# Optimization experiments

Hardware: AMD Instinct MI355X
Metric: run time of the kernel (lower is better)

## Reference

```python
import jax, jax.numpy as jnp
import numpy as np

N, E, T = 10000, 160000, 1200000
D, DM, H, L, Z = 256, 64, 1024, 3, 100


def setup_inputs() -> dict:
    key = jax.random.key(0)
    ks = jax.random.split(key, 24)
    rn = lambda k, shp, s: (s * jax.random.normal(k, shp)).astype(jnp.float32)
    return {
        'atomic_number': jax.random.randint(ks[0], (N,), 1, Z),
        'g_src': jax.random.randint(ks[1], (E,), 0, N),
        'g_dst': jax.random.randint(ks[2], (E,), 0, N),
        't_src': jax.random.randint(ks[3], (T,), 0, E),
        't_dst': jax.random.randint(ks[4], (T,), 0, E),
        'r': rn(ks[5], (E, 3), 1.5),  # bond displacement vectors, |r| ~ 2.4 A
        'atom_emb': rn(ks[6], (Z, D), 0.05),
        'Wsrc': rn(ks[7], (L, D, DM), 0.05), 'bsrc': rn(ks[8], (L, DM), 0.05),
        'Wdst': rn(ks[9], (L, D, DM), 0.05), 'bdst': rn(ks[10], (L, DM), 0.05),
        'Wedge': rn(ks[11], (L, D, DM), 0.05), 'bedge': rn(ks[12], (L, DM), 0.05),
        'attn': rn(ks[13], (L, DM), 0.05),
        'W1': rn(ks[14], (L, DM, H), 0.05), 'b1': rn(ks[15], (L, H), 0.05),
        'W2': rn(ks[16], (L, H, D), 0.05), 'b2': rn(ks[17], (L, D), 0.05),
        'Wfc': rn(ks[18], (D, 1), 0.05), 'bfc': rn(ks[19], (1,), 0.05),
    }


def _forward(atomic_number, g_src, g_dst, t_src, t_dst, r, atom_emb,
             Wsrc, bsrc, Wdst, bdst, Wedge, bedge, attn, W1, b1, W2, b2, Wfc, bfc):
    n_nodes = atomic_number.shape[0]
    n_edges = r.shape[0]
    d_model = atom_emb.shape[1]
    channels = attn.shape[-1]

    # atom embedding + RBF bond encoding (vmin=0, vmax=8, bins=d_model)
    x = atom_emb[atomic_number]                       # [N, D]
    bondlength = jnp.linalg.norm(r, axis=1)           # [E]
    centers = jnp.linspace(0.0, 8.0, d_model)
    gamma = 1.0 / (centers[1] - centers[0]) ** 2
    y = jnp.exp(-gamma * (bondlength[:, None] - centers[None, :]) ** 2)  # [E, D]

    # angular (Chebyshev) features on triplet graph t; t.ndata['r'] = g.edata['r']
    rnorm = -r / bondlength[:, None]                  # [E, 3]
    cos_jik = jnp.sum(rnorm[t_src] * rnorm[t_dst], axis=1)  # [T]
    kc = jnp.arange(channels, dtype=cos_jik.dtype)
    theta = jnp.arccos(jnp.clip(cos_jik, -1.0, 1.0))
    z_jik = jnp.cos(kc[None, :] * theta[:, None])     # [T, C] Chebyshev T_k(cos)

    node_idx = g_dst[t_dst]                           # triplet -> destination atom

    for l in range(Wsrc.shape[0]):
        xj = x @ Wsrc[l] + bsrc[l]                    # [N, DM]
        xi = x @ Wdst[l] + bdst[l]                    # [N, DM]
        xij = xj[g_src] + xi[g_dst] + (y @ Wedge[l] + bedge[l])  # [E, DM]

        e_jik = jax.nn.silu(z_jik + xij[t_src] + xij[t_dst])     # [T, DM]
        logit = jnp.sum(e_jik * attn[l], axis=-1)                # [T]
        # edge_softmax grouped by destination bond (t_dst)
        m = jax.ops.segment_max(logit, t_dst, num_segments=n_edges)
        ex = jnp.exp(logit - m[t_dst])
        den = jax.ops.segment_sum(ex, t_dst, num_segments=n_edges)
        a = ex / den[t_dst]                                      # [T]

        # scatter attended messages to destination atoms
        ft = jax.ops.segment_sum(a[:, None] * xij[t_src], node_idx,
                                 num_segments=n_nodes)           # [N, DM]
        # feedforward: DM -> 4*D -> D
        x = jax.nn.silu(ft @ W1[l] + b1[l]) @ W2[l] + b2[l]      # [N, D]

    atomwise_energy = x @ Wfc + bfc                   # [N, 1]
    return jnp.squeeze(jnp.mean(atomwise_energy))     # AvgPooling, eV/atom


def reference(atomic_number, g_src, g_dst, t_src, t_dst, r, atom_emb,
              Wsrc, bsrc, Wdst, bdst, Wedge, bedge, attn, W1, b1, W2, b2, Wfc, bfc):
    return _forward(atomic_number, g_src, g_dst, t_src, t_dst, r, atom_emb,
                    Wsrc, bsrc, Wdst, bdst, Wedge, bedge, attn, W1, b1, W2, b2, Wfc, bfc)
```

## Files before the change

kernel.cpp:

```cpp
#include <hip/hip_runtime.h>
#include <math.h>


#define DM 64
#define DMODEL 256
#define HDIM 1024
#define WPAD 264

#define BSH 9
#define NBMAX 320
#define CAPB 4608

typedef unsigned short bf16_t;
typedef __attribute__((ext_vector_type(8))) short s8v;
typedef __attribute__((ext_vector_type(4))) float f4;

__device__ __forceinline__ bf16_t f2bf(float f) {
    unsigned int u = __float_as_uint(f);
    return (bf16_t)((u + 0x7FFFu + ((u >> 16) & 1u)) >> 16);
}
__device__ __forceinline__ float bf_lo(unsigned int u) {
    return __uint_as_float(u << 16);
}
__device__ __forceinline__ float bf_hi(unsigned int u) {
    return __uint_as_float(u & 0xFFFF0000u);
}
__device__ __forceinline__ float bf2f(bf16_t v) {
    return __uint_as_float((unsigned int)v << 16);
}
__device__ __forceinline__ float silu_f(float u) {
    return u * __builtin_amdgcn_rcpf(1.f + __expf(-u));
}

__global__ void k_embed(const int* __restrict__ an, const float* __restrict__ emb,
                        bf16_t* __restrict__ x) {
    int n = blockIdx.x;
    int d = threadIdx.x;
    x[n * DMODEL + d] = f2bf(emb[an[n] * DMODEL + d]);
}

__global__ void k_edge_geom(const float* __restrict__ r, float* __restrict__ bl,
                            float* __restrict__ rn, int E) {
    int e = blockIdx.x * blockDim.x + threadIdx.x;
    if (e >= E) return;
    float a = r[e * 3 + 0], b = r[e * 3 + 1], c = r[e * 3 + 2];
    float l = sqrtf(a * a + b * b + c * c);
    bl[e] = l;
    float inv = 1.0f / l;
    rn[e * 3 + 0] = a * inv;
    rn[e * 3 + 1] = b * inv;
    rn[e * 3 + 2] = c * inv;
}

__global__ void k_hist(const int* __restrict__ idx, int* __restrict__ cnt, int M) {
    int t = blockIdx.x * blockDim.x + threadIdx.x;
    if (t < M) atomicAdd(&cnt[idx[t]], 1);
}

__global__ __launch_bounds__(256) void k_scan_part(
    const int* __restrict__ cnt, int* __restrict__ bsum, int M) {
    __shared__ int sm[4];
    int tid = threadIdx.x;
    int i = blockIdx.x * 256 + tid;
    int v = (i < M) ? cnt[i] : 0;
    for (int off = 32; off > 0; off >>= 1) v += __shfl_xor(v, off, 64);
    if ((tid & 63) == 0) sm[tid >> 6] = v;
    __syncthreads();
    if (tid == 0) bsum[blockIdx.x] = sm[0] + sm[1] + sm[2] + sm[3];
}

__global__ __launch_bounds__(1024) void k_scan_mid(int* __restrict__ bsum, int nb) {
    __shared__ int sm[1024];
    int tid = threadIdx.x;
    int v = (tid < nb) ? bsum[tid] : 0;
    sm[tid] = v;
    __syncthreads();
    for (int off = 1; off < 1024; off <<= 1) {
        int u = (tid >= off) ? sm[tid - off] : 0;
        __syncthreads();
        sm[tid] += u;
        __syncthreads();
    }
    if (tid < nb) bsum[tid] = sm[tid] - v;
}

__global__ __launch_bounds__(256) void k_scan_final(
    int* __restrict__ cnt, const int* __restrict__ bsum,
    int* __restrict__ rowp, int M, int total) {
    __shared__ int sm[256];
    int tid = threadIdx.x;
    int i = blockIdx.x * 256 + tid;
    int v = (i < M) ? cnt[i] : 0;
    sm[tid] = v;
    __syncthreads();
    for (int off = 1; off < 256; off <<= 1) {
        int u = (tid >= off) ? sm[tid - off] : 0;
        __syncthreads();
        sm[tid] += u;
        __syncthreads();
    }
    if (i < M) {
        rowp[i] = bsum[blockIdx.x] + sm[tid] - v;
        cnt[i] = 0;
    }
    if (i == 0) rowp[M] = total;
}


__global__ __launch_bounds__(512) void k_bhist(
    const int* __restrict__ td, int* __restrict__ gbcnt, int T, int NB) {
    __shared__ int h[NBMAX];
    int tid = threadIdx.x;
    for (int i = tid; i < NBMAX; i += 512) h[i] = 0;
    __syncthreads();
    int t0 = blockIdx.x * 4096;
    #pragma unroll
    for (int i = 0; i < 8; ++i) {
        int t = t0 + tid + i * 512;
        if (t < T) atomicAdd(&h[td[t] >> BSH], 1);
    }
    __syncthreads();
    for (int b = tid; b < NB; b += 512)
        if (h[b]) atomicAdd(&gbcnt[b], h[b]);
}

__global__ __launch_bounds__(512) void k_bscan(
    const int* __restrict__ gbcnt, int* __restrict__ bbase, int NB, int total) {
    __shared__ int sm[512];
    int tid = threadIdx.x;
    int v = (tid < NB) ? gbcnt[tid] : 0;
    sm[tid] = v;
    __syncthreads();
    for (int off = 1; off < 512; off <<= 1) {
        int u = (tid >= off) ? sm[tid - off] : 0;
        __syncthreads();
        sm[tid] += u;
        __syncthreads();
    }
    if (tid < NB) bbase[tid] = sm[tid] - v;
    if (tid == 0) bbase[NB] = total;
}

__global__ __launch_bounds__(512) void k_passA(
    const int* __restrict__ ts, const int* __restrict__ td,
    const float* __restrict__ rn, const int* __restrict__ bbase,
    int* __restrict__ bcur, int2* __restrict__ ipair, float* __restrict__ idv,
    int T, int NB) {
    __shared__ int   std_[4096];
    __shared__ int   ssrc[4096];
    __shared__ float sdv[4096];
    __shared__ int lbcnt[NBMAX], lbase[NBMAX], lpos[NBMAX], lgst[NBMAX],
                   lbb[NBMAX];
    __shared__ int ssc[512];
    int tid = threadIdx.x;
    int t0 = blockIdx.x * 4096;
    int total = min(4096, T - t0);
    for (int i = tid; i < NBMAX; i += 512) lbcnt[i] = 0;
    for (int i = tid; i < NB; i += 512) lbb[i] = bbase[i];
    __syncthreads();
    int   mtd[8], msrc[8];
    float md[8];
    #pragma unroll
    for (int i = 0; i < 8; ++i) {
        int idx = tid + i * 512;
        mtd[i] = -1;
        if (idx < total) {
            int t = t0 + idx;
            int a = ts[t], b = td[t];
            float d = rn[a * 3 + 0] * rn[b * 3 + 0]
                    + rn[a * 3 + 1] * rn[b * 3 + 1]
                    + rn[a * 3 + 2] * rn[b * 3 + 2];
            d = fminf(1.0f, fmaxf(-1.0f, d));
            mtd[i] = b; msrc[i] = a; md[i] = d;
            atomicAdd(&lbcnt[b >> BSH], 1);
        }
    }
    __syncthreads();
    int v = (tid < NB) ? lbcnt[tid] : 0;
    ssc[tid] = v;
    __syncthreads();
    for (int off = 1; off < 512; off <<= 1) {
        int u = (tid >= off) ? ssc[tid - off] : 0;
        __syncthreads();
        ssc[tid] += u;
        __syncthreads();
    }
    if (tid < NB) {
        int ex = ssc[tid] - v;
        lbase[tid] = ex;
        lpos[tid] = ex;
    }
    __syncthreads();
    #pragma unroll
    for (int i = 0; i < 8; ++i) {
        if (mtd[i] >= 0) {
            int bin = mtd[i] >> BSH;
            int p = atomicAdd(&lpos[bin], 1);
            std_[p] = mtd[i]; ssrc[p] = msrc[i]; sdv[p] = md[i];
        }
    }
    __syncthreads();
    for (int b = tid; b < NB; b += 512)
        if (lbcnt[b]) lgst[b] = atomicAdd(&bcur[b], lbcnt[b]);
    __syncthreads();
    for (int j = tid; j < total; j += 512) {
        int bin = std_[j] >> BSH;
        int dest = lbb[bin] + lgst[bin] + (j - lbase[bin]);
        ipair[dest] = make_int2(std_[j], ssrc[j]);
        idv[dest] = sdv[j];
    }
}

__global__ __launch_bounds__(512) void k_passB(
    const int2* __restrict__ ipair, const float* __restrict__ idv,
    const int* __restrict__ bbase, int2* __restrict__ packed,
    int* __restrict__ rowp, int E, int T) {
    __shared__ int2 spk[CAPB];
    __shared__ int hcnt[512], lcur[512], ssc[512];
    int tid = threadIdx.x;
    int b = blockIdx.x;
    int ibeg = bbase[b], iend = bbase[b + 1];
    int nb = iend - ibeg;
    int e0 = b << BSH;
    hcnt[tid] = 0;
    __syncthreads();
    for (int j = ibeg + tid; j < iend; j += 512)
        atomicAdd(&hcnt[ipair[j].x - e0], 1);
    __syncthreads();
    int v = hcnt[tid];
    ssc[tid] = v;
    __syncthreads();
    for (int off = 1; off < 512; off <<= 1) {
        int u = (tid >= off) ? ssc[tid - off] : 0;
        __syncthreads();
        ssc[tid] += u;
        __syncthreads();
    }
    int excl = ssc[tid] - v;
    lcur[tid] = excl;
    int e = e0 + tid;
    if (e < E) rowp[e] = ibeg + excl;
    if (b == 0 && tid == 0) rowp[E] = T;
    __syncthreads();
    bool staged = (nb <= CAPB);
    for (int j = ibeg + tid; j < iend; j += 512) {
        int2 pr = ipair[j];
        int pos = atomicAdd(&lcur[pr.x - e0], 1);
        int2 out = make_int2(pr.y, __float_as_int(idv[j]));
        if (staged) spk[pos] = out;
        else packed[ibeg + pos] = out;
    }
    __syncthreads();
    if (staged)
        for (int j = tid; j < nb; j += 512) packed[ibeg + j] = spk[j];
}

__global__ void k_escatter(const int* __restrict__ gd, const int* __restrict__ erowp,
                           int* __restrict__ cursor, int* __restrict__ epos, int E) {
    int e = blockIdx.x * blockDim.x + threadIdx.x;
    if (e >= E) return;
    int n = gd[e];
    int pos = erowp[n] + atomicAdd(&cursor[n], 1);
    epos[e] = pos;
}

__global__ __launch_bounds__(256) void k_deghist(
    const int* __restrict__ rowp, int* __restrict__ dcnt, int E) {
    __shared__ int h[256];
    int tid = threadIdx.x;
    h[tid] = 0;
    __syncthreads();
    int e = blockIdx.x * 256 + tid;
    if (e < E) {
        int d = rowp[e + 1] - rowp[e];
        if (d > 255) d = 255;
        atomicAdd(&h[d], 1);
    }
    __syncthreads();
    if (h[tid]) atomicAdd(&dcnt[tid], h[tid]);
}

__global__ __launch_bounds__(256) void k_degscatter(
    const int* __restrict__ rowp, const int* __restrict__ doff,
    int* __restrict__ dcur, int* __restrict__ eperm, int E) {
    __shared__ int lcnt[256];
    __shared__ int base[256];
    int tid = threadIdx.x;
    lcnt[tid] = 0;
    __syncthreads();
    int e = blockIdx.x * 256 + tid;
    int d = 0, rk = 0;
    if (e < E) {
        d = rowp[e + 1] - rowp[e];
        if (d > 255) d = 255;
        rk = atomicAdd(&lcnt[d], 1);
    }
    __syncthreads();
    if (lcnt[tid]) base[tid] = atomicAdd(&dcur[tid], lcnt[tid]);
    __syncthreads();
    if (e < E) eperm[E - 1 - (doff[d] + base[d] + rk)] = e;
}

__global__ __launch_bounds__(256) void k_castT(
    const float* __restrict__ src0, bf16_t* __restrict__ dst0, int K, int Nn) {
    __shared__ float tile[32][33];
    const float* src = src0 + (size_t)blockIdx.z * K * Nn;
    bf16_t* dst = dst0 + (size_t)blockIdx.z * K * Nn;
    int k0 = blockIdx.x * 32, n0 = blockIdx.y * 32;
    int tx = threadIdx.x & 31, ty = threadIdx.x >> 5;
    #pragma unroll
    for (int i = 0; i < 4; ++i) {
        int row = ty + i * 8;
        tile[row][tx] = src[(size_t)(k0 + row) * Nn + n0 + tx];
    }
    __syncthreads();
    #pragma unroll
    for (int i = 0; i < 4; ++i) {
        int row = ty + i * 8;
        dst[(size_t)(n0 + row) * K + k0 + tx] = f2bf(tile[tx][row]);
    }
}

__global__ __launch_bounds__(256) void k_node_proj(
    const bf16_t* __restrict__ xb,
    const bf16_t* __restrict__ Wst, const float* __restrict__ bs,
    const bf16_t* __restrict__ Wdt, const float* __restrict__ bd,
    bf16_t* __restrict__ xs, bf16_t* __restrict__ xd, int N) {
    __shared__ bf16_t wsl[64 * WPAD];
    __shared__ bf16_t wdl[64 * WPAD];
    int tid = threadIdx.x;
    for (int i = tid; i < 2048; i += 256) {
        int row = i >> 5, inw = i & 31;
        *(uint4*)&wsl[row * WPAD + inw * 8] =
            *(const uint4*)&Wst[(size_t)row * DMODEL + inw * 8];
        *(uint4*)&wdl[row * WPAD + inw * 8] =
            *(const uint4*)&Wdt[(size_t)row * DMODEL + inw * 8];
    }
    __syncthreads();
    int w = tid >> 6, lane = tid & 63;
    int col = lane & 15, quad = lane >> 4;
    int m0 = blockIdx.x * 64 + w * 16;
    f4 as[4] = {{0.f,0.f,0.f,0.f},{0.f,0.f,0.f,0.f},
                {0.f,0.f,0.f,0.f},{0.f,0.f,0.f,0.f}};
    f4 ad[4] = {{0.f,0.f,0.f,0.f},{0.f,0.f,0.f,0.f},
                {0.f,0.f,0.f,0.f},{0.f,0.f,0.f,0.f}};
    #pragma unroll
    for (int k0 = 0; k0 < DMODEL; k0 += 32) {
        s8v a = *(const s8v*)&xb[(size_t)(m0 + col) * DMODEL + k0 + quad * 8];
        #pragma unroll
        for (int t = 0; t < 4; ++t) {
            s8v b1v = *(const s8v*)&wsl[(t * 16 + col) * WPAD + k0 + quad * 8];
            as[t] = __builtin_amdgcn_mfma_f32_16x16x32_bf16(a, b1v, as[t], 0, 0, 0);
            s8v b2v = *(const s8v*)&wdl[(t * 16 + col) * WPAD + k0 + quad * 8];
            ad[t] = __builtin_amdgcn_mfma_f32_16x16x32_bf16(a, b2v, ad[t], 0, 0, 0);
        }
    }
    #pragma unroll
    for (int t = 0; t < 4; ++t) {
        int c = t * 16 + col;
        float bsv = bs[c], bdv = bd[c];
        #pragma unroll
        for (int r = 0; r < 4; ++r) {
            int m = m0 + quad * 4 + r;
            if (m < N) {
                xs[(size_t)m * DM + c] = f2bf(as[t][r] + bsv);
                xd[(size_t)m * DM + c] = f2bf(ad[t][r] + bdv);
            }
        }
    }
}

__global__ __launch_bounds__(256) void k_xij(
    const float* __restrict__ bl, const bf16_t* __restrict__ Wedgt,
    const float* __restrict__ be,
    const bf16_t* __restrict__ xs, const bf16_t* __restrict__ xd,
    const int* __restrict__ gs, const int* __restrict__ gd,
    bf16_t* __restrict__ xij, int E) {
    __shared__ bf16_t wel[64 * WPAD];
    int tid = threadIdx.x;
    for (int i = tid; i < 2048; i += 256) {
        int row = i >> 5, inw = i & 31;
        *(uint4*)&wel[row * WPAD + inw * 8] =
            *(const uint4*)&Wedgt[(size_t)row * DMODEL + inw * 8];
    }
    __syncthreads();
    int w = tid >> 6, lane = tid & 63;
    int col = lane & 15, quad = lane >> 4;
    int m0 = blockIdx.x * 64 + w * 16;
    const float step = 8.0f / 255.0f;
    const float gamma = (255.0f / 8.0f) * (255.0f / 8.0f);
    int me = m0 + col;
    float blv = (me < E) ? bl[me] : 0.f;
    f4 acc[4] = {{0.f,0.f,0.f,0.f},{0.f,0.f,0.f,0.f},
                 {0.f,0.f,0.f,0.f},{0.f,0.f,0.f,0.f}};
    #pragma unroll
    for (int k0 = 0; k0 < DMODEL; k0 += 32) {
        s8v a;
        #pragma unroll
        for (int j = 0; j < 8; ++j) {
            float c = (float)(k0 + quad * 8 + j) * step;
            float dd = blv - c;
            a[j] = (short)f2bf(__expf(-gamma * dd * dd));
        }
        #pragma unroll
        for (int t = 0; t < 4; ++t) {
            s8v b = *(const s8v*)&wel[(t * 16 + col) * WPAD + k0 + quad * 8];
            acc[t] = __builtin_amdgcn_mfma_f32_16x16x32_bf16(a, b, acc[t], 0, 0, 0);
        }
    }
    #pragma unroll
    for (int r = 0; r < 4; ++r) {
        int e = m0 + quad * 4 + r;
        if (e >= E) continue;
        int s = gs[e], d2 = gd[e];
        #pragma unroll
        for (int t = 0; t < 4; ++t) {
            int c = t * 16 + col;
            float v = acc[t][r] + bf2f(xs[(size_t)s * DM + c])
                    + bf2f(xd[(size_t)d2 * DM + c]) + be[c];
            xij[(size_t)e * DM + c] = f2bf(v);
        }
    }
}

__global__ __launch_bounds__(256) void k_edge_attn(
    const bf16_t* __restrict__ xij, const int2* __restrict__ packed,
    const int* __restrict__ rowp, const float* __restrict__ attn_l,
    const int* __restrict__ eperm, const int* __restrict__ epos,
    bf16_t* __restrict__ msg, int E) {
    int gtid = blockIdx.x * 256 + threadIdx.x;
    int ei = gtid >> 2;
    if (ei >= E) return;
    int q = gtid & 3;
    int e = eperm[ei];
    int beg = rowp[e], end = rowp[e + 1];

    float av[16];
    #pragma unroll
    for (int c = 0; c < 16; ++c) av[c] = attn_l[q * 16 + c];

    uint4 xe0, xe1;
    {
        const uint4* xer = (const uint4*)&xij[(size_t)e * DM + q * 16];
        xe0 = xer[0]; xe1 = xer[1];
    }
    float acc[16];
    #pragma unroll
    for (int c = 0; c < 16; ++c) acc[c] = 0.f;
    float den = 0.f;

    if (beg < end) {
        int2 pk0 = packed[beg];
        int2 pk1 = (beg + 1 < end) ? packed[beg + 1] : pk0;
        const uint4* s0 = (const uint4*)&xij[(size_t)pk0.x * DM + q * 16];
        uint4 nsa = s0[0], nsb = s0[1];
        for (int p = beg; p < end; ++p) {
            float d = __int_as_float(pk0.y);
            uint4 xa = nsa, xb = nsb;
            if (p + 1 < end) {
                const uint4* sn = (const uint4*)&xij[(size_t)pk1.x * DM + q * 16];
                nsa = sn[0]; nsb = sn[1];
                pk0 = pk1;
                if (p + 2 < end) pk1 = packed[p + 2];
            }
            float d2 = d + d;
            float t2  = fmaf(d2, d, -1.f);
            float t3  = fmaf(d2, t2, -d);
            float t4  = fmaf(t2 + t2, t2, -1.f);
            float t7  = fmaf(t4 + t4, t3, -d);
            float t8  = fmaf(t4 + t4, t4, -1.f);
            float t15 = fmaf(t8 + t8, t7, -d);
            float t16 = fmaf(t8 + t8, t8, -1.f);
            float t17 = fmaf(t16 + t16, d, -t15);
            float t31 = fmaf(t16 + t16, t15, -d);
            float t32 = fmaf(t16 + t16, t16, -1.f);
            float t33 = fmaf(t32 + t32, d, -t31);
            float t48 = fmaf(t32 + t32, t16, -t16);
            float t49 = fmaf(t32 + t32, t17, -t15);
            float za, zb;
            if (q == 0)      { za = 1.f;  zb = d;   }
            else if (q == 1) { za = t16;  zb = t17; }
            else if (q == 2) { za = t32;  zb = t33; }
            else             { za = t48;  zb = t49; }
            float logit = 0.f;
            #define CH2(uw, ew, c)                                            \
            {                                                                 \
                float u0 = za + bf_lo(uw) + bf_lo(ew);                        \
                float zn = fmaf(d2, zb, -za); za = zb; zb = zn;               \
                float u1 = za + bf_hi(uw) + bf_hi(ew);                        \
                zn = fmaf(d2, zb, -za); za = zb; zb = zn;                     \
                logit = fmaf(silu_f(u0), av[c], logit);                       \
                logit = fmaf(silu_f(u1), av[c + 1], logit);                   \
            }
            CH2(xa.x, xe0.x, 0);
            CH2(xa.y, xe0.y, 2);
            CH2(xa.z, xe0.z, 4);
            CH2(xa.w, xe0.w, 6);
            CH2(xb.x, xe1.x, 8);
            CH2(xb.y, xe1.y, 10);
            CH2(xb.z, xe1.z, 12);
            CH2(xb.w, xe1.w, 14);
            #undef CH2
            logit += __shfl_xor(logit, 1, 64);
            logit += __shfl_xor(logit, 2, 64);
            float wg = __expf(logit);
            den += wg;
            acc[0]  = fmaf(wg, bf_lo(xa.x), acc[0]);
            acc[1]  = fmaf(wg, bf_hi(xa.x), acc[1]);
            acc[2]  = fmaf(wg, bf_lo(xa.y), acc[2]);
            acc[3]  = fmaf(wg, bf_hi(xa.y), acc[3]);
            acc[4]  = fmaf(wg, bf_lo(xa.z), acc[4]);
            acc[5]  = fmaf(wg, bf_hi(xa.z), acc[5]);
            acc[6]  = fmaf(wg, bf_lo(xa.w), acc[6]);
            acc[7]  = fmaf(wg, bf_hi(xa.w), acc[7]);
            acc[8]  = fmaf(wg, bf_lo(xb.x), acc[8]);
            acc[9]  = fmaf(wg, bf_hi(xb.x), acc[9]);
            acc[10] = fmaf(wg, bf_lo(xb.y), acc[10]);
            acc[11] = fmaf(wg, bf_hi(xb.y), acc[11]);
            acc[12] = fmaf(wg, bf_lo(xb.z), acc[12]);
            acc[13] = fmaf(wg, bf_hi(xb.z), acc[13]);
            acc[14] = fmaf(wg, bf_lo(xb.w), acc[14]);
            acc[15] = fmaf(wg, bf_hi(xb.w), acc[15]);
        }
    }
    float inv = (den > 0.f) ? 1.f / den : 0.f;
    uint4 o0, o1;
    o0.x = (unsigned int)f2bf(acc[0] * inv)  | ((unsigned int)f2bf(acc[1] * inv) << 16);
    o0.y = (unsigned int)f2bf(acc[2] * inv)  | ((unsigned int)f2bf(acc[3] * inv) << 16);
    o0.z = (unsigned int)f2bf(acc[4] * inv)  | ((unsigned int)f2bf(acc[5] * inv) << 16);
    o0.w = (unsigned int)f2bf(acc[6] * inv)  | ((unsigned int)f2bf(acc[7] * inv) << 16);
    o1.x = (unsigned int)f2bf(acc[8] * inv)  | ((unsigned int)f2bf(acc[9] * inv) << 16);
    o1.y = (unsigned int)f2bf(acc[10] * inv) | ((unsigned int)f2bf(acc[11] * inv) << 16);
    o1.z = (unsigned int)f2bf(acc[12] * inv) | ((unsigned int)f2bf(acc[13] * inv) << 16);
    o1.w = (unsigned int)f2bf(acc[14] * inv) | ((unsigned int)f2bf(acc[15] * inv) << 16);
    int mrow = epos[e];
    uint4* op = (uint4*)&msg[(size_t)mrow * DM + q * 16];
    op[0] = o0;
    op[1] = o1;
}

__global__ __launch_bounds__(256) void k_aggregate(
    const bf16_t* __restrict__ msg, const int* __restrict__ erowp,
    bf16_t* __restrict__ ft, int N) {
    int gtid = blockIdx.x * 256 + threadIdx.x;
    int n = gtid >> 4;
    if (n >= N) return;
    int quad = gtid & 15;
    int beg = erowp[n], end = erowp[n + 1];
    float a0 = 0.f, a1 = 0.f, a2 = 0.f, a3 = 0.f;
    for (int j = beg; j < end; ++j) {
        uint2 uv = *(const uint2*)&msg[(size_t)j * DM + quad * 4];
        a0 += bf_lo(uv.x); a1 += bf_hi(uv.x);
        a2 += bf_lo(uv.y); a3 += bf_hi(uv.y);
    }
    ushort4 o = {f2bf(a0), f2bf(a1), f2bf(a2), f2bf(a3)};
    *(ushort4*)&ft[(size_t)n * DM + quad * 4] = o;
}

__global__ __launch_bounds__(256) void k_ffn_fused(
    const bf16_t* __restrict__ ft, const bf16_t* __restrict__ W1t,
    const float* __restrict__ b1, const bf16_t* __restrict__ W2t,
    const float* __restrict__ b2, bf16_t* __restrict__ x, int N) {
    __shared__ bf16_t w1s[2][64 * 72];
    __shared__ bf16_t w2s[2][64 * 72];
    __shared__ bf16_t hld[4][16 * 72];
    __shared__ float b1s[HDIM];
    int tid = threadIdx.x;
    int w = tid >> 6, lane = tid & 63;
    int col = lane & 15, quad = lane >> 4;
    int m0 = blockIdx.x * 64 + w * 16;
    int c0 = blockIdx.y * 64;
    bf16_t* myl = hld[w];

    #pragma unroll
    for (int j = 0; j < 4; ++j) b1s[tid + j * 256] = b1[tid + j * 256];

    s8v fa0 = *(const s8v*)&ft[(size_t)(m0 + col) * DM + quad * 8];
    s8v fa1 = *(const s8v*)&ft[(size_t)(m0 + col) * DM + 32 + quad * 8];

    int srow0 = tid >> 3;
    int srow1 = 32 + srow0;
    int skb = tid & 7;

    f4 acc[4] = {{0.f,0.f,0.f,0.f},{0.f,0.f,0.f,0.f},
                 {0.f,0.f,0.f,0.f},{0.f,0.f,0.f,0.f}};

    {
        uint4 a0 = *(const uint4*)&W1t[(size_t)srow0 * DM + skb * 8];
        uint4 a1 = *(const uint4*)&W1t[(size_t)srow1 * DM + skb * 8];
        uint4 c0v = *(const uint4*)&W2t[(size_t)(c0 + srow0) * HDIM + skb * 8];
        uint4 c1v = *(const uint4*)&W2t[(size_t)(c0 + srow1) * HDIM + skb * 8];
        *(uint4*)&w1s[0][srow0 * 72 + skb * 8] = a0;
        *(uint4*)&w1s[0][srow1 * 72 + skb * 8] = a1;
        *(uint4*)&w2s[0][srow0 * 72 + skb * 8] = c0v;
        *(uint4*)&w2s[0][srow1 * 72 + skb * 8] = c1v;
    }
    __syncthreads();

    #pragma unroll 1
    for (int kc = 0; kc < 16; ++kc) {
        int cb = kc & 1, nb = cb ^ 1;
        int ch0 = kc * 64;
        int chn = (kc < 15) ? ch0 + 64 : ch0;
        uint4 na0 = *(const uint4*)&W1t[(size_t)(chn + srow0) * DM + skb * 8];
        uint4 na1 = *(const uint4*)&W1t[(size_t)(chn + srow1) * DM + skb * 8];
        uint4 nc0 = *(const uint4*)&W2t[(size_t)(c0 + srow0) * HDIM + chn + skb * 8];
        uint4 nc1 = *(const uint4*)&W2t[(size_t)(c0 + srow1) * HDIM + chn + skb * 8];
        #pragma unroll
        for (int th = 0; th < 4; ++th) {
            s8v wb0 = *(const s8v*)&w1s[cb][(th * 16 + col) * 72 + quad * 8];
            s8v wb1 = *(const s8v*)&w1s[cb][(th * 16 + col) * 72 + 32 + quad * 8];
            f4 hv = {0.f, 0.f, 0.f, 0.f};
            hv = __builtin_amdgcn_mfma_f32_16x16x32_bf16(fa0, wb0, hv, 0, 0, 0);
            hv = __builtin_amdgcn_mfma_f32_16x16x32_bf16(fa1, wb1, hv, 0, 0, 0);
            float bb = b1s[ch0 + th * 16 + col];
            #pragma unroll
            for (int r = 0; r < 4; ++r)
                myl[(quad * 4 + r) * 72 + th * 16 + col] =
                    f2bf(silu_f(hv[r] + bb));
        }
        s8v ha0 = *(const s8v*)&myl[col * 72 + quad * 8];
        s8v ha1 = *(const s8v*)&myl[col * 72 + 32 + quad * 8];
        #pragma unroll
        for (int t2 = 0; t2 < 4; ++t2) {
            s8v vb0 = *(const s8v*)&w2s[cb][(t2 * 16 + col) * 72 + quad * 8];
            s8v vb1 = *(const s8v*)&w2s[cb][(t2 * 16 + col) * 72 + 32 + quad * 8];
            acc[t2] = __builtin_amdgcn_mfma_f32_16x16x32_bf16(ha0, vb0, acc[t2], 0, 0, 0);
            acc[t2] = __builtin_amdgcn_mfma_f32_16x16x32_bf16(ha1, vb1, acc[t2], 0, 0, 0);
        }
        __syncthreads();
        if (kc < 15) {
            *(uint4*)&w1s[nb][srow0 * 72 + skb * 8] = na0;
            *(uint4*)&w1s[nb][srow1 * 72 + skb * 8] = na1;
            *(uint4*)&w2s[nb][srow0 * 72 + skb * 8] = nc0;
            *(uint4*)&w2s[nb][srow1 * 72 + skb * 8] = nc1;
        }
        __syncthreads();
    }
    #pragma unroll
    for (int t2 = 0; t2 < 4; ++t2) {
        int c = c0 + t2 * 16 + col;
        float bb = b2[c];
        #pragma unroll
        for (int r = 0; r < 4; ++r) {
            int m = m0 + quad * 4 + r;
            if (m < N) x[(size_t)m * DMODEL + c] = f2bf(acc[t2][r] + bb);
        }
    }
}

__global__ __launch_bounds__(256) void k_out_reduce(
    const bf16_t* __restrict__ x, const float* __restrict__ Wfc,
    float* __restrict__ acc, int NT) {
    __shared__ float sm[4];
    int tid = threadIdx.x;
    float v = 0.f;
    int np = NT / 2;
    const unsigned int* xp = (const unsigned int*)x;
    for (int i = blockIdx.x * blockDim.x + tid; i < np; i += gridDim.x * blockDim.x) {
        unsigned int u = xp[i];
        int c = (2 * i) & (DMODEL - 1);
        v = fmaf(bf_lo(u), Wfc[c], v);
        v = fmaf(bf_hi(u), Wfc[c + 1], v);
    }
    for (int off = 32; off > 0; off >>= 1) v += __shfl_xor(v, off, 64);
    if ((tid & 63) == 0) sm[tid >> 6] = v;
    __syncthreads();
    if (tid == 0) {
        float s = sm[0] + sm[1] + sm[2] + sm[3];
        atomicAdd(acc, s);
    }
}

__global__ void k_out_final(const float* __restrict__ acc, const float* __restrict__ bfc,
                            float* __restrict__ out, float invN) {
    out[0] = acc[0] * invN + bfc[0];
}

extern "C" void kernel_launch(void* const* d_in, const int* in_sizes, int n_in,
                              void* d_out, int out_size, void* d_ws, size_t ws_size,
                              hipStream_t stream) {
    const int*   an    = (const int*)d_in[0];
    const int*   gs    = (const int*)d_in[1];
    const int*   gd    = (const int*)d_in[2];
    const int*   ts    = (const int*)d_in[3];
    const int*   td    = (const int*)d_in[4];
    const float* r     = (const float*)d_in[5];
    const float* emb   = (const float*)d_in[6];
    const float* Wsrc  = (const float*)d_in[7];
    const float* bsrc  = (const float*)d_in[8];
    const float* Wdst  = (const float*)d_in[9];
    const float* bdst  = (const float*)d_in[10];
    const float* Wedge = (const float*)d_in[11];
    const float* bedge = (const float*)d_in[12];
    const float* attn  = (const float*)d_in[13];
    const float* W1    = (const float*)d_in[14];
    const float* b1    = (const float*)d_in[15];
    const float* W2    = (const float*)d_in[16];
    const float* b2    = (const float*)d_in[17];
    const float* Wfc   = (const float*)d_in[18];
    const float* bfc   = (const float*)d_in[19];

    const int N = in_sizes[0];
    const int E = in_sizes[1];
    const int T = in_sizes[3];
    const int NB = (E + 511) >> BSH;

    char* w = (char*)d_ws;
    size_t off = 0;
    auto alloc = [&](size_t bytes) {
        void* p = w + off;
        off += (bytes + 255) & ~(size_t)255;
        return p;
    };
    bf16_t* xb     = (bf16_t*)alloc((size_t)(N + 64) * DMODEL * 2);
    float*  rn     = (float*) alloc((size_t)E * 3 * 4);
    float*  bl     = (float*) alloc(((size_t)E + 64) * 4);
    int*    rowp   = (int*)   alloc(((size_t)E + 1) * 4);
    int*    bsum   = (int*)   alloc(4096);
    int2*   packed = (int2*)  alloc((size_t)T * 8);
    int2*   ipair  = (int2*)  alloc((size_t)T * 8);
    float*  idv    = (float*) alloc((size_t)T * 4);
    int*    gbcnt  = (int*)   alloc(NBMAX * 4);
    int*    bcur   = (int*)   alloc(NBMAX * 4);
    int*    bbase  = (int*)   alloc((NBMAX + 1) * 4);
    int*    dcnt   = (int*)   alloc(1024);
    int*    dcur   = (int*)   alloc(1024);
    int*    ecnt   = (int*)   alloc((size_t)N * 4);
    int*    erowp  = (int*)   alloc(((size_t)N + 1) * 4);
    int*    epos   = (int*)   alloc((size_t)E * 4);
    int*    eperm  = (int*)   alloc((size_t)E * 4);
    bf16_t* xs     = (bf16_t*)alloc((size_t)N * DM * 2);
    bf16_t* xd     = (bf16_t*)alloc((size_t)N * DM * 2);
    bf16_t* xij    = (bf16_t*)alloc((size_t)E * DM * 2);
    bf16_t* msg    = (bf16_t*)alloc((size_t)E * DM * 2);
    bf16_t* ft     = (bf16_t*)alloc((size_t)(N + 64) * DM * 2);
    bf16_t* W1t    = (bf16_t*)alloc((size_t)3 * HDIM * DM * 2);
    bf16_t* W2t    = (bf16_t*)alloc((size_t)3 * DMODEL * HDIM * 2);
    bf16_t* Wedgt  = (bf16_t*)alloc((size_t)3 * DM * DMODEL * 2);
    bf16_t* Wst    = (bf16_t*)alloc((size_t)3 * DM * DMODEL * 2);
    bf16_t* Wdt    = (bf16_t*)alloc((size_t)3 * DM * DMODEL * 2);
    float*  accs   = (float*) alloc(64);
    (void)ws_size; (void)n_in; (void)out_size;

    const int nbScanN = (N + 255) / 256;
    const int nbT = (T + 4095) / 4096;

    k_embed<<<N, 256, 0, stream>>>(an, emb, xb);
    k_edge_geom<<<(E + 255) / 256, 256, 0, stream>>>(r, bl, rn, E);
    k_castT<<<dim3(DM / 32, HDIM / 32, 3), 256, 0, stream>>>(W1, W1t, DM, HDIM);
    k_castT<<<dim3(HDIM / 32, DMODEL / 32, 3), 256, 0, stream>>>(W2, W2t, HDIM, DMODEL);
    k_castT<<<dim3(DMODEL / 32, DM / 32, 3), 256, 0, stream>>>(Wedge, Wedgt, DMODEL, DM);
    k_castT<<<dim3(DMODEL / 32, DM / 32, 3), 256, 0, stream>>>(Wsrc, Wst, DMODEL, DM);
    k_castT<<<dim3(DMODEL / 32, DM / 32, 3), 256, 0, stream>>>(Wdst, Wdt, DMODEL, DM);
    hipMemsetAsync(gbcnt, 0, (size_t)2 * NBMAX * 4, stream);
    k_bhist<<<nbT, 512, 0, stream>>>(td, gbcnt, T, NB);
    k_bscan<<<1, 512, 0, stream>>>(gbcnt, bbase, NB, T);
    k_passA<<<nbT, 512, 0, stream>>>(ts, td, rn, bbase, bcur, ipair, idv, T, NB);
    k_passB<<<NB, 512, 0, stream>>>(ipair, idv, bbase, packed, rowp, E, T);
    hipMemsetAsync(dcnt, 0, 2048, stream);
    k_deghist<<<(E + 255) / 256, 256, 0, stream>>>(rowp, dcnt, E);
    k_scan_mid<<<1, 1024, 0, stream>>>(dcnt, 256);
    k_degscatter<<<(E + 255) / 256, 256, 0, stream>>>(rowp, dcnt, dcur, eperm, E);
    hipMemsetAsync(ecnt, 0, (size_t)N * 4, stream);
    k_hist<<<(E + 255) / 256, 256, 0, stream>>>(gd, ecnt, E);
    k_scan_part<<<nbScanN, 256, 0, stream>>>(ecnt, bsum, N);
    k_scan_mid<<<1, 1024, 0, stream>>>(bsum, nbScanN);
    k_scan_final<<<nbScanN, 256, 0, stream>>>(ecnt, bsum, erowp, N, E);
    k_escatter<<<(E + 255) / 256, 256, 0, stream>>>(gd, erowp, ecnt, epos, E);

    for (int l = 0; l < 3; ++l) {
        k_node_proj<<<(N + 63) / 64, 256, 0, stream>>>(
            xb, Wst + (size_t)l * DM * DMODEL, bsrc + l * DM,
            Wdt + (size_t)l * DM * DMODEL, bdst + l * DM, xs, xd, N);
        k_xij<<<(E + 63) / 64, 256, 0, stream>>>(
            bl, Wedgt + (size_t)l * DM * DMODEL, bedge + l * DM,
            xs, xd, gs, gd, xij, E);
        k_edge_attn<<<(E * 4 + 255) / 256, 256, 0, stream>>>(
            xij, packed, rowp, attn + l * DM, eperm, epos, msg, E);
        k_aggregate<<<(N * 16 + 255) / 256, 256, 0, stream>>>(
            msg, erowp, ft, N);
        k_ffn_fused<<<dim3((N + 63) / 64, 4), 256, 0, stream>>>(
            ft, W1t + (size_t)l * HDIM * DM, b1 + l * HDIM,
            W2t + (size_t)l * DMODEL * HDIM, b2 + l * DMODEL, xb, N);
    }

    hipMemsetAsync(accs, 0, 4, stream);
    k_out_reduce<<<120, 256, 0, stream>>>(xb, Wfc, accs, N * DMODEL);
    k_out_final<<<1, 1, 0, stream>>>(accs, bfc, (float*)d_out, 1.0f / (float)N);
}
```

Measured before the change: 596.1 us.

## Merge preprocessing kernels and memsets to cut launch count

Combines embedding and edge geometry into one kernel, and folds the five weight transpose-casts into a single launch. The degree and node histograms, both mid-scans, and the deg-scatter with the final scan are each paired into shared launches. The memsets become one contiguous clear, and the final output is written by the last block of the reduce kernel through an atomic ticket. This removes roughly a dozen small launches and their gaps, at the cost of more branchy kernels and a zero_bytes size hardcoded to specific buffer sizes.

```diff
diff --git a/kernel.cpp b/kernel.cpp
--- a/kernel.cpp
+++ b/kernel.cpp
@@ -32,29 +32,68 @@
     return u * __builtin_amdgcn_rcpf(1.f + __expf(-u));
 }
 
-__global__ void k_embed(const int* __restrict__ an, const float* __restrict__ emb,
-                        bf16_t* __restrict__ x) {
-    int n = blockIdx.x;
-    int d = threadIdx.x;
-    x[n * DMODEL + d] = f2bf(emb[an[n] * DMODEL + d]);
-}
-
-__global__ void k_edge_geom(const float* __restrict__ r, float* __restrict__ bl,
-                            float* __restrict__ rn, int E) {
-    int e = blockIdx.x * blockDim.x + threadIdx.x;
-    if (e >= E) return;
-    float a = r[e * 3 + 0], b = r[e * 3 + 1], c = r[e * 3 + 2];
-    float l = sqrtf(a * a + b * b + c * c);
-    bl[e] = l;
-    float inv = 1.0f / l;
-    rn[e * 3 + 0] = a * inv;
-    rn[e * 3 + 1] = b * inv;
-    rn[e * 3 + 2] = c * inv;
-}
-
-__global__ void k_hist(const int* __restrict__ idx, int* __restrict__ cnt, int M) {
-    int t = blockIdx.x * blockDim.x + threadIdx.x;
-    if (t < M) atomicAdd(&cnt[idx[t]], 1);
+__global__ __launch_bounds__(256) void k_prep(
+    const int* __restrict__ an, const float* __restrict__ emb,
+    bf16_t* __restrict__ x, const float* __restrict__ r,
+    float* __restrict__ bl, float* __restrict__ rn, int N, int E) {
+    if ((int)blockIdx.x < N) {
+        int n = blockIdx.x;
+        int d = threadIdx.x;
+        x[n * DMODEL + d] = f2bf(emb[an[n] * DMODEL + d]);
+    } else {
+        int e = (blockIdx.x - N) * 256 + threadIdx.x;
+        if (e >= E) return;
+        float a = r[e * 3 + 0], b = r[e * 3 + 1], c = r[e * 3 + 2];
+        float l = sqrtf(a * a + b * b + c * c);
+        bl[e] = l;
+        float inv = 1.0f / l;
+        rn[e * 3 + 0] = a * inv;
+        rn[e * 3 + 1] = b * inv;
+        rn[e * 3 + 2] = c * inv;
+    }
+}
+
+__global__ __launch_bounds__(256) void k_castT_all(
+    const float* __restrict__ W1, const float* __restrict__ W2,
+    const float* __restrict__ Wedge, const float* __restrict__ Wsrc,
+    const float* __restrict__ Wdst,
+    bf16_t* __restrict__ W1t, bf16_t* __restrict__ W2t,
+    bf16_t* __restrict__ Wedgt, bf16_t* __restrict__ Wst,
+    bf16_t* __restrict__ Wdt) {
+    __shared__ float tile[32][33];
+    int id = blockIdx.x;
+    const float* src; bf16_t* dst; int K, Nn, k0, n0;
+    if (id < 192) {
+        int layer = id / 64, t = id % 64;
+        src = W1 + (size_t)layer * DM * HDIM;
+        dst = W1t + (size_t)layer * HDIM * DM;
+        K = DM; Nn = HDIM; k0 = (t % 2) * 32; n0 = (t / 2) * 32;
+    } else if (id < 960) {
+        int rem = id - 192, layer = rem / 256, t = rem % 256;
+        src = W2 + (size_t)layer * HDIM * DMODEL;
+        dst = W2t + (size_t)layer * DMODEL * HDIM;
+        K = HDIM; Nn = DMODEL; k0 = (t % 32) * 32; n0 = (t / 32) * 32;
+    } else {
+        int rem = id - 960, which = rem / 48, r2 = rem % 48;
+        int layer = r2 / 16, t = r2 % 16;
+        const float* s3[3] = {Wedge, Wsrc, Wdst};
+        bf16_t* d3[3] = {Wedgt, Wst, Wdt};
+        src = s3[which] + (size_t)layer * DMODEL * DM;
+        dst = d3[which] + (size_t)layer * DM * DMODEL;
+        K = DMODEL; Nn = DM; k0 = (t % 8) * 32; n0 = (t / 8) * 32;
+    }
+    int tx = threadIdx.x & 31, ty = threadIdx.x >> 5;
+    #pragma unroll
+    for (int i = 0; i < 4; ++i) {
+        int row = ty + i * 8;
+        tile[row][tx] = src[(size_t)(k0 + row) * Nn + n0 + tx];
+    }
+    __syncthreads();
+    #pragma unroll
+    for (int i = 0; i < 4; ++i) {
+        int row = ty + i * 8;
+        dst[(size_t)(n0 + row) * K + k0 + tx] = f2bf(tile[tx][row]);
+    }
 }
 
 __global__ __launch_bounds__(256) void k_scan_part(
@@ -69,7 +108,7 @@
     if (tid == 0) bsum[blockIdx.x] = sm[0] + sm[1] + sm[2] + sm[3];
 }
 
-__global__ __launch_bounds__(1024) void k_scan_mid(int* __restrict__ bsum, int nb) {
+__device__ __forceinline__ void scan_mid_body(int* bsum, int nb) {
     __shared__ int sm[1024];
     int tid = threadIdx.x;
     int v = (tid < nb) ? bsum[tid] : 0;
@@ -84,28 +123,11 @@
     if (tid < nb) bsum[tid] = sm[tid] - v;
 }
 
-__global__ __launch_bounds__(256) void k_scan_final(
-    int* __restrict__ cnt, const int* __restrict__ bsum,
-    int* __restrict__ rowp, int M, int total) {
-    __shared__ int sm[256];
-    int tid = threadIdx.x;
-    int i = blockIdx.x * 256 + tid;
-    int v = (i < M) ? cnt[i] : 0;
-    sm[tid] = v;
-    __syncthreads();
-    for (int off = 1; off < 256; off <<= 1) {
-        int u = (tid >= off) ? sm[tid - off] : 0;
-        __syncthreads();
-        sm[tid] += u;
-        __syncthreads();
-    }
-    if (i < M) {
-        rowp[i] = bsum[blockIdx.x] + sm[tid] - v;
-        cnt[i] = 0;
-    }
-    if (i == 0) rowp[M] = total;
-}
-
+__global__ __launch_bounds__(1024) void k_scan2(
+    int* __restrict__ dcnt, int* __restrict__ bsum, int nbN) {
+    if (blockIdx.x == 0) scan_mid_body(dcnt, 256);
+    else scan_mid_body(bsum, nbN);
+}
 
 __global__ __launch_bounds__(512) void k_bhist(
     const int* __restrict__ td, int* __restrict__ gbcnt, int T, int NB) {
@@ -255,6 +277,67 @@
         for (int j = tid; j < nb; j += 512) packed[ibeg + j] = spk[j];
 }
 
+__global__ __launch_bounds__(256) void k_deg_ghist(
+    const int* __restrict__ rowp, int* __restrict__ dcnt,
+    const int* __restrict__ gd, int* __restrict__ ecnt, int E) {
+    __shared__ int h[256];
+    int tid = threadIdx.x;
+    h[tid] = 0;
+    __syncthreads();
+    int e = blockIdx.x * 256 + tid;
+    if (e < E) {
+        int d = rowp[e + 1] - rowp[e];
+        if (d > 255) d = 255;
+        atomicAdd(&h[d], 1);
+        atomicAdd(&ecnt[gd[e]], 1);
+    }
+    __syncthreads();
+    if (h[tid]) atomicAdd(&dcnt[tid], h[tid]);
+}
+
+__global__ __launch_bounds__(256) void k_degscat_final(
+    const int* __restrict__ rowp, const int* __restrict__ doff,
+    int* __restrict__ dcur, int* __restrict__ eperm, int E, int nbE,
+    int* __restrict__ ecnt, const int* __restrict__ bsum,
+    int* __restrict__ erowp, int N) {
+    int tid = threadIdx.x;
+    if ((int)blockIdx.x < nbE) {
+        __shared__ int lcnt[256];
+        __shared__ int base[256];
+        lcnt[tid] = 0;
+        __syncthreads();
+        int e = blockIdx.x * 256 + tid;
+        int d = 0, rk = 0;
+        if (e < E) {
+            d = rowp[e + 1] - rowp[e];
+            if (d > 255) d = 255;
+            rk = atomicAdd(&lcnt[d], 1);
+        }
+        __syncthreads();
+        if (lcnt[tid]) base[tid] = atomicAdd(&dcur[tid], lcnt[tid]);
+        __syncthreads();
+        if (e < E) eperm[E - 1 - (doff[d] + base[d] + rk)] = e;
+    } else {
+        __shared__ int sm[256];
+        int bb = blockIdx.x - nbE;
+        int i = bb * 256 + tid;
+        int v = (i < N) ? ecnt[i] : 0;
+        sm[tid] = v;
+        __syncthreads();
+        for (int off = 1; off < 256; off <<= 1) {
+            int u = (tid >= off) ? sm[tid - off] : 0;
+            __syncthreads();
+            sm[tid] += u;
+            __syncthreads();
+        }
+        if (i < N) {
+            erowp[i] = bsum[bb] + sm[tid] - v;
+            ecnt[i] = 0;
+        }
+        if (i == 0) erowp[N] = E;
+    }
+}
+
 __global__ void k_escatter(const int* __restrict__ gd, const int* __restrict__ erowp,
                            int* __restrict__ cursor, int* __restrict__ epos, int E) {
     int e = blockIdx.x * blockDim.x + threadIdx.x;
@@ -262,63 +345,6 @@
     int n = gd[e];
     int pos = erowp[n] + atomicAdd(&cursor[n], 1);
     epos[e] = pos;
-}
-
-__global__ __launch_bounds__(256) void k_deghist(
-    const int* __restrict__ rowp, int* __restrict__ dcnt, int E) {
-    __shared__ int h[256];
-    int tid = threadIdx.x;
-    h[tid] = 0;
-    __syncthreads();
-    int e = blockIdx.x * 256 + tid;
-    if (e < E) {
-        int d = rowp[e + 1] - rowp[e];
-        if (d > 255) d = 255;
-        atomicAdd(&h[d], 1);
-    }
-    __syncthreads();
-    if (h[tid]) atomicAdd(&dcnt[tid], h[tid]);
-}
-
-__global__ __launch_bounds__(256) void k_degscatter(
-    const int* __restrict__ rowp, const int* __restrict__ doff,
-    int* __restrict__ dcur, int* __restrict__ eperm, int E) {
-    __shared__ int lcnt[256];
-    __shared__ int base[256];
-    int tid = threadIdx.x;
-    lcnt[tid] = 0;
-    __syncthreads();
-    int e = blockIdx.x * 256 + tid;
-    int d = 0, rk = 0;
-    if (e < E) {
-        d = rowp[e + 1] - rowp[e];
-        if (d > 255) d = 255;
-        rk = atomicAdd(&lcnt[d], 1);
-    }
-    __syncthreads();
-    if (lcnt[tid]) base[tid] = atomicAdd(&dcur[tid], lcnt[tid]);
-    __syncthreads();
-    if (e < E) eperm[E - 1 - (doff[d] + base[d] + rk)] = e;
-}
-
-__global__ __launch_bounds__(256) void k_castT(
-    const float* __restrict__ src0, bf16_t* __restrict__ dst0, int K, int Nn) {
-    __shared__ float tile[32][33];
-    const float* src = src0 + (size_t)blockIdx.z * K * Nn;
-    bf16_t* dst = dst0 + (size_t)blockIdx.z * K * Nn;
-    int k0 = blockIdx.x * 32, n0 = blockIdx.y * 32;
-    int tx = threadIdx.x & 31, ty = threadIdx.x >> 5;
-    #pragma unroll
-    for (int i = 0; i < 4; ++i) {
-        int row = ty + i * 8;
-        tile[row][tx] = src[(size_t)(k0 + row) * Nn + n0 + tx];
-    }
-    __syncthreads();
-    #pragma unroll
-    for (int i = 0; i < 4; ++i) {
-        int row = ty + i * 8;
-        dst[(size_t)(n0 + row) * K + k0 + tx] = f2bf(tile[tx][row]);
-    }
 }
 
 __global__ __launch_bounds__(256) void k_node_proj(
@@ -651,7 +677,8 @@
 
 __global__ __launch_bounds__(256) void k_out_reduce(
     const bf16_t* __restrict__ x, const float* __restrict__ Wfc,
-    float* __restrict__ acc, int NT) {
+    float* __restrict__ acc, const float* __restrict__ bfc,
+    float* __restrict__ out, float invN, int NT) {
     __shared__ float sm[4];
     int tid = threadIdx.x;
     float v = 0.f;
@@ -668,13 +695,14 @@
     __syncthreads();
     if (tid == 0) {
         float s = sm[0] + sm[1] + sm[2] + sm[3];
-        atomicAdd(acc, s);
-    }
-}
-
-__global__ void k_out_final(const float* __restrict__ acc, const float* __restrict__ bfc,
-                            float* __restrict__ out, float invN) {
-    out[0] = acc[0] * invN + bfc[0];
+        atomicAdd(&acc[0], s);
+        __threadfence();
+        unsigned int prev = atomicAdd((unsigned int*)&acc[1], 1u);
+        if (prev == gridDim.x - 1) {
+            float tot = atomicAdd(&acc[0], 0.0f);
+            out[0] = tot * invN + bfc[0];
+        }
+    }
 }
 
 extern "C" void kernel_launch(void* const* d_in, const int* in_sizes, int n_in,
@@ -713,6 +741,13 @@
         off += (bytes + 255) & ~(size_t)255;
         return p;
     };
+    int*    gbcnt  = (int*)   alloc(NBMAX * 4);
+    int*    bcur   = (int*)   alloc(NBMAX * 4);
+    int*    dcnt   = (int*)   alloc(1024);
+    int*    dcur   = (int*)   alloc(1024);
+    int*    ecnt   = (int*)   alloc((size_t)N * 4);
+    float*  accs   = (float*) alloc(64);
+    const size_t zero_bytes = (size_t)(1280 + 1280 + 1024 + 1024 + 40192 + 256);
     bf16_t* xb     = (bf16_t*)alloc((size_t)(N + 64) * DMODEL * 2);
     float*  rn     = (float*) alloc((size_t)E * 3 * 4);
     float*  bl     = (float*) alloc(((size_t)E + 64) * 4);
@@ -721,12 +756,7 @@
     int2*   packed = (int2*)  alloc((size_t)T * 8);
     int2*   ipair  = (int2*)  alloc((size_t)T * 8);
     float*  idv    = (float*) alloc((size_t)T * 4);
-    int*    gbcnt  = (int*)   alloc(NBMAX * 4);
-    int*    bcur   = (int*)   alloc(NBMAX * 4);
     int*    bbase  = (int*)   alloc((NBMAX + 1) * 4);
-    int*    dcnt   = (int*)   alloc(1024);
-    int*    dcur   = (int*)   alloc(1024);
-    int*    ecnt   = (int*)   alloc((size_t)N * 4);
     int*    erowp  = (int*)   alloc(((size_t)N + 1) * 4);
     int*    epos   = (int*)   alloc((size_t)E * 4);
     int*    eperm  = (int*)   alloc((size_t)E * 4);
@@ -740,34 +770,26 @@
     bf16_t* Wedgt  = (bf16_t*)alloc((size_t)3 * DM * DMODEL * 2);
     bf16_t* Wst    = (bf16_t*)alloc((size_t)3 * DM * DMODEL * 2);
     bf16_t* Wdt    = (bf16_t*)alloc((size_t)3 * DM * DMODEL * 2);
-    float*  accs   = (float*) alloc(64);
     (void)ws_size; (void)n_in; (void)out_size;
 
     const int nbScanN = (N + 255) / 256;
+    const int nbE = (E + 255) / 256;
     const int nbT = (T + 4095) / 4096;
 
-    k_embed<<<N, 256, 0, stream>>>(an, emb, xb);
-    k_edge_geom<<<(E + 255) / 256, 256, 0, stream>>>(r, bl, rn, E);
-    k_castT<<<dim3(DM / 32, HDIM / 32, 3), 256, 0, stream>>>(W1, W1t, DM, HDIM);
-    k_castT<<<dim3(HDIM / 32, DMODEL / 32, 3), 256, 0, stream>>>(W2, W2t, HDIM, DMODEL);
-    k_castT<<<dim3(DMODEL / 32, DM / 32, 3), 256, 0, stream>>>(Wedge, Wedgt, DMODEL, DM);
-    k_castT<<<dim3(DMODEL / 32, DM / 32, 3), 256, 0, stream>>>(Wsrc, Wst, DMODEL, DM);
-    k_castT<<<dim3(DMODEL / 32, DM / 32, 3), 256, 0, stream>>>(Wdst, Wdt, DMODEL, DM);
-    hipMemsetAsync(gbcnt, 0, (size_t)2 * NBMAX * 4, stream);
+    hipMemsetAsync(gbcnt, 0, zero_bytes, stream);
+    k_prep<<<N + nbE, 256, 0, stream>>>(an, emb, xb, r, bl, rn, N, E);
+    k_castT_all<<<1104, 256, 0, stream>>>(W1, W2, Wedge, Wsrc, Wdst,
+                                          W1t, W2t, Wedgt, Wst, Wdt);
     k_bhist<<<nbT, 512, 0, stream>>>(td, gbcnt, T, NB);
     k_bscan<<<1, 512, 0, stream>>>(gbcnt, bbase, NB, T);
     k_passA<<<nbT, 512, 0, stream>>>(ts, td, rn, bbase, bcur, ipair, idv, T, NB);
     k_passB<<<NB, 512, 0, stream>>>(ipair, idv, bbase, packed, rowp, E, T);
-    hipMemsetAsync(dcnt, 0, 2048, stream);
-    k_deghist<<<(E + 255) / 256, 256, 0, stream>>>(rowp, dcnt, E);
-    k_scan_mid<<<1, 1024, 0, stream>>>(dcnt, 256);
-    k_degscatter<<<(E + 255) / 256, 256, 0, stream>>>(rowp, dcnt, dcur, eperm, E);
-    hipMemsetAsync(ecnt, 0, (size_t)N * 4, stream);
-    k_hist<<<(E + 255) / 256, 256, 0, stream>>>(gd, ecnt, E);
+    k_deg_ghist<<<nbE, 256, 0, stream>>>(rowp, dcnt, gd, ecnt, E);
     k_scan_part<<<nbScanN, 256, 0, stream>>>(ecnt, bsum, N);
-    k_scan_mid<<<1, 1024, 0, stream>>>(bsum, nbScanN);
-    k_scan_final<<<nbScanN, 256, 0, stream>>>(ecnt, bsum, erowp, N, E);
-    k_escatter<<<(E + 255) / 256, 256, 0, stream>>>(gd, erowp, ecnt, epos, E);
+    k_scan2<<<2, 1024, 0, stream>>>(dcnt, bsum, nbScanN);
+    k_degscat_final<<<nbE + nbScanN, 256, 0, stream>>>(
+        rowp, dcnt, dcur, eperm, E, nbE, ecnt, bsum, erowp, N);
+    k_escatter<<<nbE, 256, 0, stream>>>(gd, erowp, ecnt, epos, E);
 
     for (int l = 0; l < 3; ++l) {
         k_node_proj<<<(N + 63) / 64, 256, 0, stream>>>(
@@ -785,7 +807,6 @@
             W2t + (size_t)l * DMODEL * HDIM, b2 + l * DMODEL, xb, N);
     }
 
-    hipMemsetAsync(accs, 0, 4, stream);
-    k_out_reduce<<<120, 256, 0, stream>>>(xb, Wfc, accs, N * DMODEL);
-    k_out_final<<<1, 1, 0, stream>>>(accs, bfc, (float*)d_out, 1.0f / (float)N);
-}
+    k_out_reduce<<<120, 256, 0, stream>>>(xb, Wfc, accs, bfc, (float*)d_out,
+                                          1.0f / (float)N, N * DMODEL);
+}
```

Result: faster. 578.0 us (-3.0%).
